# Kernel optimization log

Measured on AMD Instinct MI355X. Metric: run time of the kernel, lower is better.

The kernel has to match this reference:

```python
import jax, jax.numpy as jnp
import numpy as np

B, Q, L, D = 4, 600, 2048, 256
H, HD, DFF, KD = 8, 32, 2048, 32  # heads, head_dim, ffn dim, gasa kernel dim
SCALE = HD ** -0.5


def setup_inputs() -> dict:
    key = jax.random.key(0)
    ks = jax.random.split(key, 24)
    w = lambda k, shape, s=0.02: (jax.random.normal(k, shape, jnp.float32) * s)
    inp = {
        "queries": jax.random.normal(ks[0], (B, Q, D), jnp.float32),
        "memory": jax.random.normal(ks[1], (B, L, D), jnp.float32),
        "memory_pos": jax.random.normal(ks[2], (B, L, 3), jnp.float32),
        "query_pos": jax.random.normal(ks[3], (B, Q, 3), jnp.float32),
        # self-attention (nn.MultiheadAttention packed in_proj)
        "sa_in_w": w(ks[4], (3 * D, D)), "sa_in_b": jnp.zeros((3 * D,), jnp.float32),
        "sa_out_w": w(ks[5], (D, D)), "sa_out_b": jnp.zeros((D,), jnp.float32),
        "norm1_g": jnp.ones((D,), jnp.float32), "norm1_b": jnp.zeros((D,), jnp.float32),
        # cross-attention projections
        "q_w": w(ks[6], (D, D)), "q_b": jnp.zeros((D,), jnp.float32),
        "k_w": w(ks[7], (D, D)), "k_b": jnp.zeros((D,), jnp.float32),
        "v_w": w(ks[8], (D, D)), "v_b": jnp.zeros((D,), jnp.float32),
        "o_w": w(ks[9], (D, D)), "o_b": jnp.zeros((D,), jnp.float32),
        "norm2_g": jnp.ones((D,), jnp.float32), "norm2_b": jnp.zeros((D,), jnp.float32),
        # GASA geometric-bias kernel: beta, MLP 1->KD->1
        "beta": jnp.asarray(1.0, jnp.float32),
        "dk_w1": w(ks[10], (KD, 1), 0.1), "dk_b1": jnp.zeros((KD,), jnp.float32),
        "dk_w2": w(ks[11], (1, KD), 0.1), "dk_b2": jnp.full((1,), -1.0, jnp.float32),
        # FFN
        "ffn_w1": w(ks[12], (DFF, D)), "ffn_b1": jnp.zeros((DFF,), jnp.float32),
        "ffn_w2": w(ks[13], (D, DFF)), "ffn_b2": jnp.zeros((D,), jnp.float32),
        "norm3_g": jnp.ones((D,), jnp.float32), "norm3_b": jnp.zeros((D,), jnp.float32),
    }
    return inp


def _ln(x, g, b, eps=1e-5):
    m = jnp.mean(x, -1, keepdims=True)
    v = jnp.mean((x - m) ** 2, -1, keepdims=True)
    return (x - m) * jax.lax.rsqrt(v + eps) * g + b


def _heads(x, wt, b):  # x:[B,N,D] -> [B,H,N,HD]
    y = x @ wt.T + b
    return y.reshape(x.shape[0], x.shape[1], H, HD).transpose(0, 2, 1, 3)


def reference(queries, memory, memory_pos, query_pos,
              sa_in_w, sa_in_b, sa_out_w, sa_out_b, norm1_g, norm1_b,
              q_w, q_b, k_w, k_b, v_w, v_b, o_w, o_b, norm2_g, norm2_b,
              beta, dk_w1, dk_b1, dk_w2, dk_b2,
              ffn_w1, ffn_b1, ffn_w2, ffn_b2, norm3_g, norm3_b):
    # ---- self-attention (post-norm, no query_pe) ----
    wq, wk, wv = jnp.split(sa_in_w, 3, axis=0)
    bq, bk, bv = jnp.split(sa_in_b, 3)
    qh = _heads(queries, wq, bq)
    kh = _heads(queries, wk, bk)
    vh = _heads(queries, wv, bv)
    a = jax.nn.softmax(jnp.einsum('bhqd,bhkd->bhqk', qh, kh) * SCALE, axis=-1)
    sa = jnp.einsum('bhqk,bhkd->bhqd', a, vh).transpose(0, 2, 1, 3).reshape(B, Q, D)
    sa = sa @ sa_out_w.T + sa_out_b
    x = _ln(queries + sa, norm1_g, norm1_b)

    # ---- GASA cross-attention ----
    Qh = _heads(x, q_w, q_b)          # [B,H,Q,HD]
    Kh = _heads(memory, k_w, k_b)     # [B,H,L,HD]
    Vh = _heads(memory, v_w, v_b)     # [B,H,L,HD]
    # cdist + learned kernel MLP, clamp to [-10, 0] (suppress-only)
    d2 = jnp.sum((query_pos[:, :, None, :] - memory_pos[:, None, :, :]) ** 2, -1)
    dist = jnp.sqrt(jnp.maximum(d2, 0.0))                     # [B,Q,L]
    hid = jax.nn.relu(dist[..., None] * dk_w1[:, 0] + dk_b1)  # [B,Q,L,KD]
    bias = (hid @ dk_w2[0]) + dk_b2[0]                        # [B,Q,L]
    bias = jnp.clip(bias, -10.0, 0.0)
    scores = jnp.einsum('bhqd,bhkd->bhqk', Qh, Kh) * SCALE + beta * bias[:, None]
    attn = jax.nn.softmax(scores, axis=-1)
    ca = jnp.einsum('bhqk,bhkd->bhqd', attn, Vh).transpose(0, 2, 1, 3).reshape(B, Q, D)
    ca = ca @ o_w.T + o_b
    x = _ln(x + ca, norm2_g, norm2_b)

    # ---- FFN (post-norm) ----
    f = jax.nn.relu(x @ ffn_w1.T + ffn_b1) @ ffn_w2.T + ffn_b2
    return _ln(x + f, norm3_g, norm3_b)
```

## Files before the change

### kernel.cpp

```cpp
#include <hip/hip_runtime.h>
#include <hip/hip_bf16.h>

typedef __hip_bfloat16 bf16;
typedef __attribute__((ext_vector_type(8))) short  short8;
typedef __attribute__((ext_vector_type(4))) float  f32x4;

#define B_ 4
#define Q_ 600
#define L_ 2048
#define D_ 256
#define H_ 8
#define HD_ 32
#define DFF_ 2048
#define KD_ 32
#define SCALE_ 0.17677669529663687f
#define L2E_   1.4426950408889634f
#define SL2E_  (SCALE_ * L2E_)

template<int MODE>
__device__ __forceinline__ float ldx(const void* p, size_t i, bool f32)
{
    if (MODE == 0) return __bfloat162float(((const bf16*)p)[i]);
    if (MODE == 1) return ((const float*)p)[i];
    return f32 ? ((const float*)p)[i] : __bfloat162float(((const bf16*)p)[i]);
}
__device__ __forceinline__ short8 ld8_f32(const float* p)
{
    const float4 a = *(const float4*)p;
    const float4 b = *(const float4*)(p + 4);
    union { short8 s; bf16 h[8]; } u;
    u.h[0] = __float2bfloat16(a.x); u.h[1] = __float2bfloat16(a.y);
    u.h[2] = __float2bfloat16(a.z); u.h[3] = __float2bfloat16(a.w);
    u.h[4] = __float2bfloat16(b.x); u.h[5] = __float2bfloat16(b.y);
    u.h[6] = __float2bfloat16(b.z); u.h[7] = __float2bfloat16(b.w);
    return u.s;
}
template<int MODE>
__device__ __forceinline__ short8 ld8x(const void* p, size_t i, bool f32)
{
    if (MODE == 0) return *(const short8*)((const bf16*)p + i);
    if (MODE == 1) return ld8_f32((const float*)p + i);
    return f32 ? ld8_f32((const float*)p + i) : *(const short8*)((const bf16*)p + i);
}

__global__ __launch_bounds__(256)
void detect_kernel(const unsigned short* __restrict__ q, int* __restrict__ flag)
{
    __shared__ float red[4];
    const int tid = threadIdx.x;
    unsigned short u = q[tid];
    float f = __uint_as_float(((unsigned)(u & 0x7FFF)) << 16);
    if (f != f) f = 1e30f;
    #pragma unroll
    for (int o = 32; o > 0; o >>= 1) f = fmaxf(f, __shfl_xor(f, o));
    if ((tid & 63) == 0) red[tid >> 6] = f;
    __syncthreads();
    if (tid == 0) {
        float m = fmaxf(fmaxf(red[0], red[1]), fmaxf(red[2], red[3]));
        *flag = (m > 100.f) ? 1 : 0;
    }
}

template<int AM>
__device__ __forceinline__ void gemm_core(const void* __restrict__ A,
    const void* __restrict__ W, int M, int K, int kbeg, int kend,
    int bm, int bn, bool f32, bf16* As, bf16* Bs, f32x4 (&acc)[2][2])
{
    const int tid = threadIdx.x;
    const int w = tid >> 6, lane = tid & 63;
    const int quad = lane >> 4, l16 = lane & 15;
    const int wm = (w & 1) << 5, wn = (w >> 1) << 5;
    const int srow = tid >> 2, scol = (tid & 3) << 3;
    const int gma = (bm + srow < M) ? bm + srow : M - 1;

    short8 pa = ld8x<AM>(A, (size_t)gma * K + kbeg + scol, f32);
    short8 pb = ld8x<2>(W, (size_t)(bn + srow) * K + kbeg + scol, f32);

    for (int k0 = kbeg; k0 < kend; k0 += 32) {
        *(short8*)&As[srow * 40 + scol] = pa;
        *(short8*)&Bs[srow * 40 + scol] = pb;
        __syncthreads();
        if (k0 + 32 < kend) {
            pa = ld8x<AM>(A, (size_t)gma * K + k0 + 32 + scol, f32);
            pb = ld8x<2>(W, (size_t)(bn + srow) * K + k0 + 32 + scol, f32);
        }
        short8 af[2], bfr[2];
        #pragma unroll
        for (int t = 0; t < 2; t++) {
            af[t]  = *(const short8*)&As[(wm + t * 16 + l16) * 40 + quad * 8];
            bfr[t] = *(const short8*)&Bs[(wn + t * 16 + l16) * 40 + quad * 8];
        }
        #pragma unroll
        for (int mt = 0; mt < 2; mt++)
            #pragma unroll
            for (int nt = 0; nt < 2; nt++)
                acc[mt][nt] = __builtin_amdgcn_mfma_f32_16x16x32_bf16(
                    af[mt], bfr[nt], acc[mt][nt], 0, 0, 0);
        __syncthreads();
    }
}

template<int AM, int RM, int CM, bool RELU, int SPLIT>
__global__ __launch_bounds__(256)
void gemm_mfma(const void* __restrict__ A, const void* __restrict__ W,
               const void* __restrict__ bias, const void* __restrict__ R,
               void* __restrict__ C, int M, int N, int K,
               const int* __restrict__ flagp)
{
    const bool f32 = (*flagp != 0);
    __shared__ alignas(16) bf16 As[64 * 40];
    __shared__ alignas(16) bf16 Bs[64 * 40];
    const int bm = blockIdx.y << 6, bn = blockIdx.x << 6;
    const int KS = K / SPLIT, z = (SPLIT > 1) ? blockIdx.z : 0;

    f32x4 acc[2][2] = {{{0.f,0.f,0.f,0.f},{0.f,0.f,0.f,0.f}},
                       {{0.f,0.f,0.f,0.f},{0.f,0.f,0.f,0.f}}};
    gemm_core<AM>(A, W, M, K, z * KS, z * KS + KS, bm, bn, f32, As, Bs, acc);

    const int tid = threadIdx.x;
    const int w = tid >> 6, lane = tid & 63;
    const int quad = lane >> 4, l16 = lane & 15;
    const int wm = (w & 1) << 5, wn = (w >> 1) << 5;

    #pragma unroll
    for (int mt = 0; mt < 2; mt++) {
        #pragma unroll
        for (int r = 0; r < 4; r++) {
            const int row = bm + wm + mt * 16 + quad * 4 + r;
            if (row >= M) continue;
            #pragma unroll
            for (int nt = 0; nt < 2; nt++) {
                const int col = bn + wn + nt * 16 + l16;
                if (SPLIT > 1) {
                    ((float*)C)[((size_t)z * M + row) * N + col] = acc[mt][nt][r];
                } else {
                    float v = acc[mt][nt][r] + ldx<2>(bias, col, f32);
                    if (RM >= 0) v += ldx<RM < 0 ? 0 : RM>(R, (size_t)row * N + col, f32);
                    if (RELU) v = fmaxf(v, 0.f);
                    if (CM == 0) ((bf16*)C)[(size_t)row * N + col] = __float2bfloat16(v);
                    else         ((float*)C)[(size_t)row * N + col] = v;
                }
            }
        }
    }
}

__global__ __launch_bounds__(256)
void kv_proj(const void* __restrict__ A,
             const void* __restrict__ kw, const void* __restrict__ kb,
             const void* __restrict__ vw, const void* __restrict__ vb,
             bf16* __restrict__ kf, bf16* __restrict__ vf,
             int M, int K, const int* __restrict__ flagp)
{
    const bool f32 = (*flagp != 0);
    __shared__ alignas(16) bf16 As[64 * 40];
    __shared__ alignas(16) bf16 Bs[64 * 40];
    const int sel = blockIdx.x >> 2;
    const void* W  = sel ? vw : kw;
    const void* bs = sel ? vb : kb;
    bf16* C        = sel ? vf : kf;
    const int bn = (blockIdx.x & 3) << 6;
    const int bm = blockIdx.y << 6;

    f32x4 acc[2][2] = {{{0.f,0.f,0.f,0.f},{0.f,0.f,0.f,0.f}},
                       {{0.f,0.f,0.f,0.f},{0.f,0.f,0.f,0.f}}};
    gemm_core<2>(A, W, M, K, 0, K, bm, bn, f32, As, Bs, acc);

    const int tid = threadIdx.x;
    const int w = tid >> 6, lane = tid & 63;
    const int quad = lane >> 4, l16 = lane & 15;
    const int wm = (w & 1) << 5, wn = (w >> 1) << 5;
    #pragma unroll
    for (int mt = 0; mt < 2; mt++)
        #pragma unroll
        for (int r = 0; r < 4; r++) {
            const int row = bm + wm + mt * 16 + quad * 4 + r;
            if (row >= M) continue;
            #pragma unroll
            for (int nt = 0; nt < 2; nt++) {
                const int col = bn + wn + nt * 16 + l16;
                C[(size_t)row * 256 + col] =
                    __float2bfloat16(acc[mt][nt][r] + ldx<2>(bs, col, f32));
            }
        }
}

template<int RM, int OM, int S>
__global__ __launch_bounds__(64)
void red_ln(const float* __restrict__ P, const void* __restrict__ bias,
            const void* __restrict__ R, const void* __restrict__ gg,
            const void* __restrict__ bb, void* __restrict__ Y,
            int M, const int* __restrict__ flagp)
{
    const bool f32 = (*flagp != 0);
    const int row = blockIdx.x, lane = threadIdx.x;
    const int d0 = lane * 4;
    float v[4];
    {
        float4 a = *(const float4*)(P + ((size_t)0 * M + row) * D_ + d0);
        v[0] = a.x; v[1] = a.y; v[2] = a.z; v[3] = a.w;
    }
    #pragma unroll
    for (int s = 1; s < S; s++) {
        float4 a = *(const float4*)(P + ((size_t)s * M + row) * D_ + d0);
        v[0] += a.x; v[1] += a.y; v[2] += a.z; v[3] += a.w;
    }
    #pragma unroll
    for (int j = 0; j < 4; j++)
        v[j] += ldx<2>(bias, d0 + j, f32) + ldx<RM>(R, (size_t)row * D_ + d0 + j, f32);

    float s1 = v[0] + v[1] + v[2] + v[3];
    float s2 = v[0]*v[0] + v[1]*v[1] + v[2]*v[2] + v[3]*v[3];
    #pragma unroll
    for (int o = 32; o > 0; o >>= 1) {
        s1 += __shfl_xor(s1, o);
        s2 += __shfl_xor(s2, o);
    }
    const float mean = s1 * (1.f / D_);
    const float var = s2 * (1.f / D_) - mean * mean;
    const float rinv = rsqrtf(var + 1e-5f);
    float o[4];
    #pragma unroll
    for (int j = 0; j < 4; j++)
        o[j] = (v[j] - mean) * rinv * ldx<2>(gg, d0 + j, f32) + ldx<2>(bb, d0 + j, f32);
    const size_t i = (size_t)row * D_ + d0;
    if (OM == 1 || (OM == 2 && f32)) {
        float4 t{o[0], o[1], o[2], o[3]};
        *(float4*)((float*)Y + i) = t;
    } else {
        bf16* y = (bf16*)Y + i;
        y[0] = __float2bfloat16(o[0]); y[1] = __float2bfloat16(o[1]);
        y[2] = __float2bfloat16(o[2]); y[3] = __float2bfloat16(o[3]);
    }
}

template<bool HASBIAS, int NSEG>
__global__ __launch_bounds__(256)
void flash_attn(const bf16* __restrict__ Qm, int qs,
                const bf16* __restrict__ Km, int ks,
                const bf16* __restrict__ Vm, int vs,
                const bf16* __restrict__ biasg,
                bf16* __restrict__ ctx, bf16* __restrict__ pO,
                float* __restrict__ pml, int NQ, int LK)
{
    __shared__ alignas(16) bf16 Ksh[64 * 40];
    __shared__ alignas(16) bf16 Vt[32 * 72];
    __shared__ alignas(16) bf16 Psh[64 * 72];
    __shared__ alignas(16) bf16 Bsh[HASBIAS ? 64 * 72 : 8];

    const int tid = threadIdx.x;
    const int w = tid >> 6, lane = tid & 63;
    const int quad = lane >> 4, l16 = lane & 15;
    const int b = blockIdx.z & 3, seg = blockIdx.z >> 2;
    const int h = blockIdx.y, q0 = blockIdx.x * 64;
    const int segLen = LK / NSEG;
    const int lbeg = seg * segLen, lend = lbeg + segLen;

    int qrow = q0 + w * 16 + l16; if (qrow > NQ - 1) qrow = NQ - 1;
    const short8 aq = *(const short8*)(Qm + (size_t)(b * NQ + qrow) * qs + h * HD_ + quad * 8);

    f32x4 O0 = {0.f, 0.f, 0.f, 0.f}, O1 = {0.f, 0.f, 0.f, 0.f};
    float mi[4] = {-3e38f, -3e38f, -3e38f, -3e38f};
    float li[4] = {0.f, 0.f, 0.f, 0.f};

    const int srow = tid >> 2, sc4 = tid & 3;
    const int nch = (segLen + 63) >> 6;

    for (int ch = 0; ch < nch; ch++) {
        const int l0 = lbeg + (ch << 6);
        {
            int lg = l0 + srow; if (lg > LK - 1) lg = LK - 1;
            short8 k8 = *(const short8*)(Km + (size_t)(b * LK + lg) * ks + h * HD_ + sc4 * 8);
            *(short8*)&Ksh[srow * 40 + sc4 * 8] = k8;
            short8 v8 = *(const short8*)(Vm + (size_t)(b * LK + lg) * vs + h * HD_ + sc4 * 8);
            const int swc = srow ^ (sc4 * 16);
            #pragma unroll
            for (int j = 0; j < 8; j++)
                Vt[(sc4 * 8 + j) * 72 + swc] = ((const bf16*)&v8)[j];
            if (HASBIAS) {
                #pragma unroll
                for (int rep = 0; rep < 2; rep++) {
                    int chid = tid + rep * 256;
                    int br = chid >> 3, bc = chid & 7;
                    int qg = q0 + br; if (qg > NQ - 1) qg = NQ - 1;
                    *(short8*)&Bsh[br * 72 + bc * 8] =
                        *(const short8*)(biasg + (size_t)(b * NQ + qg) * LK + l0 + bc * 8);
                }
            }
        }
        __syncthreads();

        f32x4 sv[4];
        #pragma unroll
        for (int jt = 0; jt < 4; jt++) {
            short8 kb = *(const short8*)&Ksh[(jt * 16 + l16) * 40 + quad * 8];
            sv[jt] = __builtin_amdgcn_mfma_f32_16x16x32_bf16(aq, kb, (f32x4){0.f,0.f,0.f,0.f}, 0, 0, 0);
        }
        float tv[4][4];
        #pragma unroll
        for (int jt = 0; jt < 4; jt++) {
            const bool valid = (l0 + jt * 16 + l16) < lend;
            #pragma unroll
            for (int r = 0; r < 4; r++) {
                float t = sv[jt][r] * SL2E_;
                if (HASBIAS)
                    t += L2E_ * __bfloat162float(Bsh[(w * 16 + quad * 4 + r) * 72 + jt * 16 + l16]);
                tv[jt][r] = valid ? t : -3e38f;
            }
        }
        #pragma unroll
        for (int r = 0; r < 4; r++) {
            float cm = fmaxf(fmaxf(tv[0][r], tv[1][r]), fmaxf(tv[2][r], tv[3][r]));
            cm = fmaxf(cm, __shfl_xor(cm, 1));
            cm = fmaxf(cm, __shfl_xor(cm, 2));
            cm = fmaxf(cm, __shfl_xor(cm, 4));
            cm = fmaxf(cm, __shfl_xor(cm, 8));
            const float m2 = fmaxf(mi[r], cm);
            const float al = exp2f(mi[r] - m2);
            mi[r] = m2;
            O0[r] *= al; O1[r] *= al;
            float rs = 0.f;
            #pragma unroll
            for (int jt = 0; jt < 4; jt++) {
                float p = exp2f(tv[jt][r] - m2);
                rs += p;
                Psh[(w * 16 + quad * 4 + r) * 72 + jt * 16 + l16] = __float2bfloat16(p);
            }
            rs += __shfl_xor(rs, 1);
            rs += __shfl_xor(rs, 2);
            rs += __shfl_xor(rs, 4);
            rs += __shfl_xor(rs, 8);
            li[r] = li[r] * al + rs;
        }
        const int sw0 = 16 * (l16 >> 3);
        const int sw1 = 16 * (2 + (l16 >> 3));
        #pragma unroll
        for (int kt = 0; kt < 2; kt++) {
            short8 ap  = *(const short8*)&Psh[(w * 16 + l16) * 72 + kt * 32 + quad * 8];
            short8 bv0 = *(const short8*)&Vt[(l16) * 72 + ((kt * 32 + quad * 8) ^ sw0)];
            short8 bv1 = *(const short8*)&Vt[(16 + l16) * 72 + ((kt * 32 + quad * 8) ^ sw1)];
            O0 = __builtin_amdgcn_mfma_f32_16x16x32_bf16(ap, bv0, O0, 0, 0, 0);
            O1 = __builtin_amdgcn_mfma_f32_16x16x32_bf16(ap, bv1, O1, 0, 0, 0);
        }
        __syncthreads();
    }

    #pragma unroll
    for (int r = 0; r < 4; r++) {
        const int qg = q0 + w * 16 + quad * 4 + r;
        if (qg >= NQ) continue;
        const float inv = 1.f / li[r];
        const size_t rowp = (size_t)(blockIdx.z * 8 + h) * NQ + qg;
        bf16* op = pO + rowp * 32;
        op[l16]      = __float2bfloat16(O0[r] * inv);
        op[16 + l16] = __float2bfloat16(O1[r] * inv);
        if (l16 == 0) { pml[rowp * 2 + 0] = mi[r]; pml[rowp * 2 + 1] = li[r]; }
    }
}

template<int NSEG>
__global__ __launch_bounds__(256)
void attn_combine(const bf16* __restrict__ pO, const float* __restrict__ pml,
                  bf16* __restrict__ ctx, int NQ)
{
    const int t = blockIdx.x * 256 + threadIdx.x;
    const int row = t >> 5, d = t & 31;
    const int stride = 32 * NQ;
    float ms[NSEG], ls[NSEG];
    float M = -3e38f;
    #pragma unroll
    for (int s = 0; s < NSEG; s++) {
        ms[s] = pml[(size_t)(s * stride + row) * 2 + 0];
        ls[s] = pml[(size_t)(s * stride + row) * 2 + 1];
        M = fmaxf(M, ms[s]);
    }
    float W = 0.f, acc = 0.f;
    #pragma unroll
    for (int s = 0; s < NSEG; s++) {
        float wgt = ls[s] * exp2f(ms[s] - M);
        W += wgt;
        acc += wgt * __bfloat162float(pO[(size_t)(s * stride + row) * 32 + d]);
    }
    const int bh = row / NQ, q = row - bh * NQ;
    ctx[((size_t)((bh >> 3) * NQ + q)) * D_ + (bh & 7) * HD_ + d] = __float2bfloat16(acc / W);
}

__global__ __launch_bounds__(256)
void bias_pre(const void* __restrict__ qp, const void* __restrict__ mp,
              const void* __restrict__ w1, const void* __restrict__ b1,
              const void* __restrict__ w2, const void* __restrict__ b2,
              const void* __restrict__ betap, bf16* __restrict__ out,
              const int* __restrict__ flagp)
{
    const bool f32 = (*flagp != 0);
    __shared__ float sw1[KD_], sb1[KD_], sw2[KD_], scst[2];
    const int tid = threadIdx.x;
    if (tid < KD_) {
        sw1[tid] = ldx<2>(w1, tid, f32);
        sb1[tid] = ldx<2>(b1, tid, f32);
        sw2[tid] = ldx<2>(w2, tid, f32);
    }
    if (tid == 0) { scst[0] = ldx<2>(b2, 0, f32); scst[1] = ldx<2>(betap, 0, f32); }
    __syncthreads();
    const int idx = blockIdx.x * 256 + tid;
    const int lo = (idx & 255) * 8;
    const int tq = idx >> 8;
    const int q = tq % Q_, b = tq / Q_;
    const float qx = ldx<2>(qp, (size_t)(b * Q_ + q) * 3 + 0, f32);
    const float qy = ldx<2>(qp, (size_t)(b * Q_ + q) * 3 + 1, f32);
    const float qz = ldx<2>(qp, (size_t)(b * Q_ + q) * 3 + 2, f32);
    union { short8 s; bf16 h[8]; } res;
    #pragma unroll
    for (int j = 0; j < 8; j++) {
        const int l = lo + j;
        float dx = qx - ldx<2>(mp, (size_t)(b * L_ + l) * 3 + 0, f32);
        float dy = qy - ldx<2>(mp, (size_t)(b * L_ + l) * 3 + 1, f32);
        float dz = qz - ldx<2>(mp, (size_t)(b * L_ + l) * 3 + 2, f32);
        float dist = sqrtf(dx * dx + dy * dy + dz * dz);
        float acc = scst[0];
        #pragma unroll
        for (int k = 0; k < KD_; k++)
            acc += fmaxf(dist * sw1[k] + sb1[k], 0.f) * sw2[k];
        acc = fminf(fmaxf(acc, -10.f), 0.f);
        res.h[j] = __float2bfloat16(scst[1] * acc);
    }
    *(short8*)(out + (size_t)(b * Q_ + q) * L_ + lo) = res.s;
}

extern "C" void kernel_launch(void* const* d_in, const int* in_sizes, int n_in,
                              void* d_out, int out_size, void* d_ws, size_t ws_size,
                              hipStream_t stream)
{
    const void* queries   = d_in[0];
    const void* memory    = d_in[1];
    const void* memory_pos= d_in[2];
    const void* query_pos = d_in[3];
    const void* sa_in_w   = d_in[4];
    const void* sa_in_b   = d_in[5];
    const void* sa_out_w  = d_in[6];
    const void* sa_out_b  = d_in[7];
    const void* norm1_g   = d_in[8];
    const void* norm1_b   = d_in[9];
    const void* q_w  = d_in[10], *q_b  = d_in[11];
    const void* k_w  = d_in[12], *k_b  = d_in[13];
    const void* v_w  = d_in[14], *v_b  = d_in[15];
    const void* o_w  = d_in[16], *o_b  = d_in[17];
    const void* norm2_g = d_in[18], *norm2_b = d_in[19];
    const void* beta  = d_in[20];
    const void* dk_w1 = d_in[21], *dk_b1 = d_in[22];
    const void* dk_w2 = d_in[23], *dk_b2 = d_in[24];
    const void* ffn_w1 = d_in[25], *ffn_b1 = d_in[26];
    const void* ffn_w2 = d_in[27], *ffn_b2 = d_in[28];
    const void* norm3_g = d_in[29], *norm3_b = d_in[30];

    char* base = (char*)d_ws;
    bf16*  kf     = (bf16*)(base + 0);
    bf16*  vf     = (bf16*)(base + 4194304);
    float* x1     = (float*)(base + 8388608);
    bf16*  qproj  = (bf16*)(base + 10846208);
    bf16*  cactx  = (bf16*)(base + 12075008);
    float* x2     = (float*)(base + 13303808);
    bf16*  biasw  = (bf16*)(base + 15761408);
    bf16*  qkv    = (bf16*)(base + 0);
    bf16*  sactx  = (bf16*)(base + 3686400);
    bf16*  selfO  = (bf16*)(base + 4915200);
    float* selfML = (float*)(base + 7372800);
    float* P3     = (float*)(base + 15761408);
    bf16*  crossO = (bf16*)(base + 25591808);
    float* crossML= (float*)(base + 30507008);
    float* P10    = (float*)(base + 0);
    bf16*  ffnh   = (bf16*)(base + 15761408);
    float* P13    = (float*)(base + 0);
    int*   flag   = (int*)(base + 31121408);

    const dim3 blk(256);

    detect_kernel<<<1, 256, 0, stream>>>((const unsigned short*)queries, flag);
    gemm_mfma<2, -1, 0, false, 1><<<dim3(12, 38), blk, 0, stream>>>(
        queries, sa_in_w, sa_in_b, nullptr, qkv, 2400, 768, 256, flag);
    flash_attn<false, 2><<<dim3(10, H_, 8), blk, 0, stream>>>(
        qkv, 768, qkv + 256, 768, qkv + 512, 768, nullptr,
        nullptr, selfO, selfML, 600, 600);
    attn_combine<2><<<2400, blk, 0, stream>>>(selfO, selfML, sactx, 600);
    gemm_mfma<0, -1, 1, false, 2><<<dim3(4, 38, 2), blk, 0, stream>>>(
        sactx, sa_out_w, nullptr, nullptr, P3, 2400, 256, 256, flag);
    red_ln<2, 1, 2><<<2400, 64, 0, stream>>>(
        P3, sa_out_b, queries, norm1_g, norm1_b, x1, 2400, flag);
    gemm_mfma<1, -1, 0, false, 1><<<dim3(4, 38), blk, 0, stream>>>(
        x1, q_w, q_b, nullptr, qproj, 2400, 256, 256, flag);
    kv_proj<<<dim3(8, 128), blk, 0, stream>>>(
        memory, k_w, k_b, v_w, v_b, kf, vf, 8192, 256, flag);
    bias_pre<<<2400, blk, 0, stream>>>(
        query_pos, memory_pos, dk_w1, dk_b1, dk_w2, dk_b2, beta, biasw, flag);
    flash_attn<true, 4><<<dim3(10, H_, 16), blk, 0, stream>>>(
        qproj, 256, kf, 256, vf, 256, biasw,
        nullptr, crossO, crossML, 600, 2048);
    attn_combine<4><<<2400, blk, 0, stream>>>(crossO, crossML, cactx, 600);
    gemm_mfma<0, -1, 1, false, 2><<<dim3(4, 38, 2), blk, 0, stream>>>(
        cactx, o_w, nullptr, nullptr, P10, 2400, 256, 256, flag);
    red_ln<1, 1, 2><<<2400, 64, 0, stream>>>(
        P10, o_b, x1, norm2_g, norm2_b, x2, 2400, flag);
    gemm_mfma<1, -1, 0, true, 1><<<dim3(32, 38), blk, 0, stream>>>(
        x2, ffn_w1, ffn_b1, nullptr, ffnh, 2400, 2048, 256, flag);
    gemm_mfma<0, -1, 1, false, 4><<<dim3(4, 38, 4), blk, 0, stream>>>(
        ffnh, ffn_w2, nullptr, nullptr, P13, 2400, 256, 2048, flag);
    red_ln<1, 2, 4><<<2400, 64, 0, stream>>>(
        P13, ffn_b2, x2, norm3_g, norm3_b, d_out, 2400, flag);
}
```

Baseline: 316.7 us.

## Transpose bias layout, compute row sums via MFMA, remap attention grid for head locality

```diff
diff --git a/kernel.cpp b/kernel.cpp
--- a/kernel.cpp
+++ b/kernel.cpp
@@ -3,6 +3,7 @@
 
 typedef __hip_bfloat16 bf16;
 typedef __attribute__((ext_vector_type(8))) short  short8;
+typedef __attribute__((ext_vector_type(4))) short  short4v;
 typedef __attribute__((ext_vector_type(4))) float  f32x4;
 
 #define B_ 4
@@ -239,29 +240,39 @@
 void flash_attn(const bf16* __restrict__ Qm, int qs,
                 const bf16* __restrict__ Km, int ks,
                 const bf16* __restrict__ Vm, int vs,
-                const bf16* __restrict__ biasg,
-                bf16* __restrict__ ctx, bf16* __restrict__ pO,
-                float* __restrict__ pml, int NQ, int LK)
+                const bf16* __restrict__ biasT,
+                bf16* __restrict__ pO, float* __restrict__ pml,
+                int NQ, int LK)
 {
     __shared__ alignas(16) bf16 Ksh[64 * 40];
-    __shared__ alignas(16) bf16 Vt[32 * 72];
+    __shared__ alignas(16) bf16 Vt[48 * 72];
     __shared__ alignas(16) bf16 Psh[64 * 72];
     __shared__ alignas(16) bf16 Bsh[HASBIAS ? 64 * 72 : 8];
 
     const int tid = threadIdx.x;
     const int w = tid >> 6, lane = tid & 63;
     const int quad = lane >> 4, l16 = lane & 15;
-    const int b = blockIdx.z & 3, seg = blockIdx.z >> 2;
-    const int h = blockIdx.y, q0 = blockIdx.x * 64;
+
+    const int id = blockIdx.x;
+    const int g  = ((id >> 6) << 3) + (id & 7);
+    const int h  = (id >> 3) & 7;
+    const int qt = g % 10;
+    const int zz = g / 10;
+    const int b = zz & 3, seg = zz >> 2;
+    const int q0 = qt * 64;
     const int segLen = LK / NSEG;
     const int lbeg = seg * segLen, lend = lbeg + segLen;
 
+    for (int i = tid; i < 16 * 72; i += 256) {
+        int rr = 32 + i / 72, cc = i % 72;
+        Vt[rr * 72 + cc] = __float2bfloat16(rr == 32 ? 1.f : 0.f);
+    }
+
     int qrow = q0 + w * 16 + l16; if (qrow > NQ - 1) qrow = NQ - 1;
     const short8 aq = *(const short8*)(Qm + (size_t)(b * NQ + qrow) * qs + h * HD_ + quad * 8);
 
-    f32x4 O0 = {0.f, 0.f, 0.f, 0.f}, O1 = {0.f, 0.f, 0.f, 0.f};
+    f32x4 O0 = {0.f,0.f,0.f,0.f}, O1 = {0.f,0.f,0.f,0.f}, O2 = {0.f,0.f,0.f,0.f};
     float mi[4] = {-3e38f, -3e38f, -3e38f, -3e38f};
-    float li[4] = {0.f, 0.f, 0.f, 0.f};
 
     const int srow = tid >> 2, sc4 = tid & 3;
     const int nch = (segLen + 63) >> 6;
@@ -281,10 +292,11 @@
                 #pragma unroll
                 for (int rep = 0; rep < 2; rep++) {
                     int chid = tid + rep * 256;
-                    int br = chid >> 3, bc = chid & 7;
-                    int qg = q0 + br; if (qg > NQ - 1) qg = NQ - 1;
-                    *(short8*)&Bsh[br * 72 + bc * 8] =
-                        *(const short8*)(biasg + (size_t)(b * NQ + qg) * LK + l0 + bc * 8);
+                    int ll = chid >> 3, qc = chid & 7;
+                    int qread = q0 + qc * 8;
+                    if (qread > NQ - 8) qread = NQ - 8;
+                    *(short8*)&Bsh[ll * 72 + qc * 8] =
+                        *(const short8*)(biasT + ((size_t)(b * LK) + l0 + ll) * Q_ + qread);
                 }
             }
         }
@@ -297,15 +309,27 @@
             sv[jt] = __builtin_amdgcn_mfma_f32_16x16x32_bf16(aq, kb, (f32x4){0.f,0.f,0.f,0.f}, 0, 0, 0);
         }
         float tv[4][4];
-        #pragma unroll
-        for (int jt = 0; jt < 4; jt++) {
-            const bool valid = (l0 + jt * 16 + l16) < lend;
-            #pragma unroll
-            for (int r = 0; r < 4; r++) {
-                float t = sv[jt][r] * SL2E_;
-                if (HASBIAS)
-                    t += L2E_ * __bfloat162float(Bsh[(w * 16 + quad * 4 + r) * 72 + jt * 16 + l16]);
-                tv[jt][r] = valid ? t : -3e38f;
+        if (l0 + 64 <= lend) {
+            #pragma unroll
+            for (int jt = 0; jt < 4; jt++) {
+                if (HASBIAS) {
+                    short4v bb = *(const short4v*)&Bsh[(jt * 16 + l16) * 72 + w * 16 + quad * 4];
+                    #pragma unroll
+                    for (int r = 0; r < 4; r++)
+                        tv[jt][r] = sv[jt][r] * SL2E_ + __bfloat162float(((const bf16*)&bb)[r]);
+                } else {
+                    #pragma unroll
+                    for (int r = 0; r < 4; r++)
+                        tv[jt][r] = sv[jt][r] * SL2E_;
+                }
+            }
+        } else {
+            #pragma unroll
+            for (int jt = 0; jt < 4; jt++) {
+                const bool valid = (l0 + jt * 16 + l16) < lend;
+                #pragma unroll
+                for (int r = 0; r < 4; r++)
+                    tv[jt][r] = valid ? sv[jt][r] * SL2E_ : -3e38f;
             }
         }
         #pragma unroll
@@ -318,19 +342,11 @@
             const float m2 = fmaxf(mi[r], cm);
             const float al = exp2f(mi[r] - m2);
             mi[r] = m2;
-            O0[r] *= al; O1[r] *= al;
-            float rs = 0.f;
-            #pragma unroll
-            for (int jt = 0; jt < 4; jt++) {
-                float p = exp2f(tv[jt][r] - m2);
-                rs += p;
-                Psh[(w * 16 + quad * 4 + r) * 72 + jt * 16 + l16] = __float2bfloat16(p);
-            }
-            rs += __shfl_xor(rs, 1);
-            rs += __shfl_xor(rs, 2);
-            rs += __shfl_xor(rs, 4);
-            rs += __shfl_xor(rs, 8);
-            li[r] = li[r] * al + rs;
+            O0[r] *= al; O1[r] *= al; O2[r] *= al;
+            #pragma unroll
+            for (int jt = 0; jt < 4; jt++)
+                Psh[(w * 16 + quad * 4 + r) * 72 + jt * 16 + l16] =
+                    __float2bfloat16(exp2f(tv[jt][r] - m2));
         }
         const int sw0 = 16 * (l16 >> 3);
         const int sw1 = 16 * (2 + (l16 >> 3));
@@ -339,8 +355,10 @@
             short8 ap  = *(const short8*)&Psh[(w * 16 + l16) * 72 + kt * 32 + quad * 8];
             short8 bv0 = *(const short8*)&Vt[(l16) * 72 + ((kt * 32 + quad * 8) ^ sw0)];
             short8 bv1 = *(const short8*)&Vt[(16 + l16) * 72 + ((kt * 32 + quad * 8) ^ sw1)];
+            short8 bon = *(const short8*)&Vt[(32 + l16) * 72 + kt * 32 + quad * 8];
             O0 = __builtin_amdgcn_mfma_f32_16x16x32_bf16(ap, bv0, O0, 0, 0, 0);
             O1 = __builtin_amdgcn_mfma_f32_16x16x32_bf16(ap, bv1, O1, 0, 0, 0);
+            O2 = __builtin_amdgcn_mfma_f32_16x16x32_bf16(ap, bon, O2, 0, 0, 0);
         }
         __syncthreads();
     }
@@ -349,12 +367,13 @@
     for (int r = 0; r < 4; r++) {
         const int qg = q0 + w * 16 + quad * 4 + r;
         if (qg >= NQ) continue;
-        const float inv = 1.f / li[r];
-        const size_t rowp = (size_t)(blockIdx.z * 8 + h) * NQ + qg;
+        const float li = __shfl(O2[r], lane & 48);
+        const float inv = 1.f / li;
+        const size_t rowp = (size_t)(((seg * 4 + b) * 8) + h) * NQ + qg;
         bf16* op = pO + rowp * 32;
         op[l16]      = __float2bfloat16(O0[r] * inv);
         op[16 + l16] = __float2bfloat16(O1[r] * inv);
-        if (l16 == 0) { pml[rowp * 2 + 0] = mi[r]; pml[rowp * 2 + 1] = li[r]; }
+        if (l16 == 0) { pml[rowp * 2 + 0] = mi[r]; pml[rowp * 2 + 1] = O2[r]; }
     }
 }
 
@@ -400,22 +419,23 @@
         sb1[tid] = ldx<2>(b1, tid, f32);
         sw2[tid] = ldx<2>(w2, tid, f32);
     }
-    if (tid == 0) { scst[0] = ldx<2>(b2, 0, f32); scst[1] = ldx<2>(betap, 0, f32); }
+    if (tid == 0) { scst[0] = ldx<2>(b2, 0, f32); scst[1] = L2E_ * ldx<2>(betap, 0, f32); }
     __syncthreads();
     const int idx = blockIdx.x * 256 + tid;
-    const int lo = (idx & 255) * 8;
-    const int tq = idx >> 8;
-    const int q = tq % Q_, b = tq / Q_;
-    const float qx = ldx<2>(qp, (size_t)(b * Q_ + q) * 3 + 0, f32);
-    const float qy = ldx<2>(qp, (size_t)(b * Q_ + q) * 3 + 1, f32);
-    const float qz = ldx<2>(qp, (size_t)(b * Q_ + q) * 3 + 2, f32);
+    const int q8 = idx % 75;
+    const int t2 = idx / 75;
+    const int l = t2 % L_, b = t2 / L_;
+    const int q0 = q8 * 8;
+    const float mx = ldx<2>(mp, (size_t)(b * L_ + l) * 3 + 0, f32);
+    const float my = ldx<2>(mp, (size_t)(b * L_ + l) * 3 + 1, f32);
+    const float mz = ldx<2>(mp, (size_t)(b * L_ + l) * 3 + 2, f32);
     union { short8 s; bf16 h[8]; } res;
     #pragma unroll
     for (int j = 0; j < 8; j++) {
-        const int l = lo + j;
-        float dx = qx - ldx<2>(mp, (size_t)(b * L_ + l) * 3 + 0, f32);
-        float dy = qy - ldx<2>(mp, (size_t)(b * L_ + l) * 3 + 1, f32);
-        float dz = qz - ldx<2>(mp, (size_t)(b * L_ + l) * 3 + 2, f32);
+        const int q = q0 + j;
+        float dx = ldx<2>(qp, (size_t)(b * Q_ + q) * 3 + 0, f32) - mx;
+        float dy = ldx<2>(qp, (size_t)(b * Q_ + q) * 3 + 1, f32) - my;
+        float dz = ldx<2>(qp, (size_t)(b * Q_ + q) * 3 + 2, f32) - mz;
         float dist = sqrtf(dx * dx + dy * dy + dz * dz);
         float acc = scst[0];
         #pragma unroll
@@ -424,7 +444,7 @@
         acc = fminf(fmaxf(acc, -10.f), 0.f);
         res.h[j] = __float2bfloat16(scst[1] * acc);
     }
-    *(short8*)(out + (size_t)(b * Q_ + q) * L_ + lo) = res.s;
+    *(short8*)(out + ((size_t)(b * L_) + l) * Q_ + q0) = res.s;
 }
 
 extern "C" void kernel_launch(void* const* d_in, const int* in_sizes, int n_in,
@@ -460,7 +480,7 @@
     bf16*  qproj  = (bf16*)(base + 10846208);
     bf16*  cactx  = (bf16*)(base + 12075008);
     float* x2     = (float*)(base + 13303808);
-    bf16*  biasw  = (bf16*)(base + 15761408);
+    bf16*  biasT  = (bf16*)(base + 15761408);
     bf16*  qkv    = (bf16*)(base + 0);
     bf16*  sactx  = (bf16*)(base + 3686400);
     bf16*  selfO  = (bf16*)(base + 4915200);
@@ -478,9 +498,9 @@
     detect_kernel<<<1, 256, 0, stream>>>((const unsigned short*)queries, flag);
     gemm_mfma<2, -1, 0, false, 1><<<dim3(12, 38), blk, 0, stream>>>(
         queries, sa_in_w, sa_in_b, nullptr, qkv, 2400, 768, 256, flag);
-    flash_attn<false, 2><<<dim3(10, H_, 8), blk, 0, stream>>>(
+    flash_attn<false, 2><<<640, blk, 0, stream>>>(
         qkv, 768, qkv + 256, 768, qkv + 512, 768, nullptr,
-        nullptr, selfO, selfML, 600, 600);
+        selfO, selfML, 600, 600);
     attn_combine<2><<<2400, blk, 0, stream>>>(selfO, selfML, sactx, 600);
     gemm_mfma<0, -1, 1, false, 2><<<dim3(4, 38, 2), blk, 0, stream>>>(
         sactx, sa_out_w, nullptr, nullptr, P3, 2400, 256, 256, flag);
@@ -491,10 +511,10 @@
     kv_proj<<<dim3(8, 128), blk, 0, stream>>>(
         memory, k_w, k_b, v_w, v_b, kf, vf, 8192, 256, flag);
     bias_pre<<<2400, blk, 0, stream>>>(
-        query_pos, memory_pos, dk_w1, dk_b1, dk_w2, dk_b2, beta, biasw, flag);
-    flash_attn<true, 4><<<dim3(10, H_, 16), blk, 0, stream>>>(
-        qproj, 256, kf, 256, vf, 256, biasw,
-        nullptr, crossO, crossML, 600, 2048);
+        query_pos, memory_pos, dk_w1, dk_b1, dk_w2, dk_b2, beta, biasT, flag);
+    flash_attn<true, 4><<<1280, blk, 0, stream>>>(
+        qproj, 256, kf, 256, vf, 256, biasT,
+        crossO, crossML, 600, 2048);
     attn_combine<4><<<2400, blk, 0, stream>>>(crossO, crossML, cactx, 600);
     gemm_mfma<0, -1, 1, false, 2><<<dim3(4, 38, 2), blk, 0, stream>>>(
         cactx, o_w, nullptr, nullptr, P10, 2400, 256, 256, flag);
```

Result: faster. 306.5 us (-3.2%).
